# Kernel optimization log

Hardware: AMD Instinct MI355X
Metric: run time of the kernel (lower is better)

## Reference

```python
import jax, jax.numpy as jnp
import numpy as np

TSTEPS = 64
NEU_IN = 8192
NEU_OUT = 8192
DECAY = (2.0**4 - 1.0) / 2.0**4  # hyp.decay = 4 -> 0.9375
THRES = 1.0                      # hyp.mempot_thres


def setup_inputs() -> dict:
    key = jax.random.key(0)
    k1, k2 = jax.random.split(key)
    # input spike raster over all timesteps (sparse boolean events)
    spikes_in = jax.random.bernoulli(k1, 0.2, (TSTEPS, NEU_IN))
    # kaiming_normal_ init: std = sqrt(2 / fan_in)
    std = np.sqrt(2.0 / NEU_IN).astype(np.float32)
    weights = jax.random.normal(k2, (NEU_OUT, NEU_IN), dtype=jnp.float32) * std
    return {"spikes_in": spikes_in, "weights": weights}


def reference(spikes_in, weights):
    """LIF neuron layer scanned over timesteps.

    Per step (matches torch forward):
      mempot += W @ spikes_in[t]
      spike   = mempot >= THRES
      mempot -= THRES * spike
      mempot *= where(spike, 1, DECAY)
    Returns (spikes [TSTEPS+1, NEU_OUT] bool, final mempot [NEU_OUT]).
    """
    spikes_f = spikes_in.astype(jnp.float32)

    def step(mempot, s_in):
        m = mempot + weights @ s_in                      # GEMV [NEU_OUT]
        spike = m >= THRES
        sf = spike.astype(jnp.float32)
        m = (m - THRES * sf) * jnp.where(spike, 1.0, DECAY)
        return m, spike

    m0 = jnp.zeros((NEU_OUT,), jnp.float32)
    mempot_final, spikes = jax.lax.scan(step, m0, spikes_f)
    # torch stores into self.spikes[tstep + 1]; row 0 stays zero
    spikes_out = jnp.concatenate(
        [jnp.zeros((1, NEU_OUT), dtype=bool), spikes], axis=0
    )
    return spikes_out, mempot_final
```

## Files before the change

kernel.cpp:

```cpp
#include <hip/hip_runtime.h>

#define TSTEPS 64
#define NI 8192
#define NO 8192
#define KS 16
#define KCH (NI / KS)
#define DECAY 0.9375f

typedef __attribute__((ext_vector_type(8))) short bf16x8;
typedef __attribute__((ext_vector_type(4))) float f32x4;

__global__ __launch_bounds__(256) void convert_kernel(const void* sp,
                                                      unsigned short* __restrict__ Sbf) {
    __shared__ int any;
    if (threadIdx.x == 0) any = 0;
    __syncthreads();
    int local = 0;
    const unsigned int* win = (const unsigned int*)sp;
    #pragma unroll
    for (int i = 0; i < 4; ++i) {
        unsigned int v = win[threadIdx.x * 4 + i];
        if (v & 0xFFFFFF00u) local = 1;
    }
    if (local) atomicOr(&any, 1);
    __syncthreads();
    const int f = any;

    const int gid = blockIdx.x * 256 + threadIdx.x;
    const int t   = gid >> 10;
    const int k0  = (gid & 1023) * 8;
    unsigned h[8];
    #pragma unroll
    for (int e = 0; e < 8; ++e) {
        int gi = t * NI + k0 + e;
        bool b;
        if (f) b = ((const unsigned char*)sp)[gi] != 0;
        else   b = ((const int*)sp)[gi] != 0;
        h[e] = b ? 0x3F80u : 0u;
    }
    uint4 v;
    v.x = h[0] | (h[1] << 16);
    v.y = h[2] | (h[3] << 16);
    v.z = h[4] | (h[5] << 16);
    v.w = h[6] | (h[7] << 16);
    *(uint4*)(Sbf + (size_t)t * NI + k0) = v;
}

__device__ __forceinline__ void split3(const float4& x, const float4& y,
                                       bf16x8& hi, bf16x8& mid, bf16x8& lo) {
    float v[8] = {x.x, x.y, x.z, x.w, y.x, y.y, y.z, y.w};
    #pragma unroll
    for (int e = 0; e < 8; ++e) {
        unsigned b   = __float_as_uint(v[e]);
        unsigned hb  = b & 0xFFFF0000u;
        float    r1  = v[e] - __uint_as_float(hb);
        unsigned r1b = __float_as_uint(r1);
        unsigned mb  = r1b & 0xFFFF0000u;
        float    r2  = r1 - __uint_as_float(mb);
        unsigned r2b = __float_as_uint(r2);
        unsigned lr  = (r2b + 0x7FFFu + ((r2b >> 16) & 1u)) >> 16;
        hi[e]  = (short)(b >> 16);
        mid[e] = (short)(mb >> 16);
        lo[e]  = (short)lr;
    }
}

__device__ __forceinline__ void gload_lds16(const float* g, float* l) {
    __builtin_amdgcn_global_load_lds(
        (const __attribute__((address_space(1))) void*)g,
        (__attribute__((address_space(3))) void*)l, 16, 0, 0);
}

#define MFMA_BF16 __builtin_amdgcn_mfma_f32_16x16x32_bf16
#define WAIT8() do { asm volatile("s_waitcnt vmcnt(8)" ::: "memory"); \
                     __builtin_amdgcn_sched_barrier(0); } while (0)

__global__ __launch_bounds__(256, 4) void gemm_kernel(const float* __restrict__ W,
                                                      const unsigned short* __restrict__ Sbf,
                                                      float* __restrict__ partial) {
    __shared__ __align__(1024) float lds[8192];

    const int lane = threadIdx.x & 63;
    const int w    = threadIdx.x >> 6;
    const int ob   = blockIdx.x & 63;
    const int kb   = blockIdx.x >> 6;
    const int r16  = lane & 15;
    const int kg   = lane >> 4;
    const int o0   = ob * 128 + w * 32;
    const int kblk = kb * KCH;

    char* wlds = (char*)lds + w * 8192;

    const float* gw[2][2];
    #pragma unroll
    for (int m = 0; m < 2; ++m)
        #pragma unroll
        for (int j = 0; j < 2; ++j) {
            int row  = m * 16 + j * 8 + (lane >> 3);
            int usrc = (lane & 7) ^ ((lane >> 3) & 7);
            gw[m][j] = W + (size_t)(o0 + row) * NI + kblk + usrc * 4;
        }

    int offA[2][2];
    #pragma unroll
    for (int m = 0; m < 2; ++m)
        #pragma unroll
        for (int h = 0; h < 2; ++h)
            offA[m][h] = m * 2048 + r16 * 128 + (((kg * 2 + h) ^ (r16 & 7)) * 16);

    const unsigned short* bp[4];
    #pragma unroll
    for (int n = 0; n < 4; ++n)
        bp[n] = Sbf + (size_t)(n * 16 + r16) * NI + kblk + kg * 8;

    f32x4 acc[2][4];
    #pragma unroll
    for (int m = 0; m < 2; ++m)
        #pragma unroll
        for (int n = 0; n < 4; ++n) acc[m][n] = (f32x4)0.f;

    bf16x8 bX[4], bY[4];

    #define ISSUE_A(cc, stage) do {                                          \
        char* _d = wlds + (stage) * 4096;                                    \
        _Pragma("unroll") for (int m = 0; m < 2; ++m)                        \
        _Pragma("unroll") for (int j = 0; j < 2; ++j)                        \
            gload_lds16(gw[m][j] + (cc) * 32,                                \
                        (float*)(_d + m * 2048 + j * 1024));                 \
    } while (0)

    #define ISSUE_B(BB, cc) do {                                             \
        _Pragma("unroll") for (int n = 0; n < 4; ++n)                        \
            BB[n] = *(const bf16x8*)(bp[n] + (cc) * 32);                     \
    } while (0)

    #define COMPUTE(stage, BB) do {                                          \
        const char* _s = wlds + (stage) * 4096;                              \
        _Pragma("unroll") for (int m = 0; m < 2; ++m) {                      \
            float4 a0 = *(const float4*)(_s + offA[m][0]);                   \
            float4 a1 = *(const float4*)(_s + offA[m][1]);                   \
            bf16x8 hi, mid, lo;                                              \
            split3(a0, a1, hi, mid, lo);                                     \
            _Pragma("unroll") for (int n = 0; n < 4; ++n) {                  \
                acc[m][n] = MFMA_BF16(hi,  BB[n], acc[m][n], 0, 0, 0);       \
                acc[m][n] = MFMA_BF16(mid, BB[n], acc[m][n], 0, 0, 0);       \
                acc[m][n] = MFMA_BF16(lo,  BB[n], acc[m][n], 0, 0, 0);       \
            }                                                                \
        }                                                                    \
    } while (0)

    ISSUE_A(0, 0); ISSUE_B(bX, 0);
    ISSUE_A(1, 1); ISSUE_B(bY, 1);

    #pragma unroll 1
    for (int c = 0; c < 16; c += 2) {
        WAIT8();
        COMPUTE(0, bX);
        ISSUE_A((c + 2) & 15, 0); ISSUE_B(bX, (c + 2) & 15);
        WAIT8();
        COMPUTE(1, bY);
        ISSUE_A((c + 3) & 15, 1); ISSUE_B(bY, (c + 3) & 15);
    }

    #pragma unroll
    for (int m = 0; m < 2; ++m)
        #pragma unroll
        for (int n = 0; n < 4; ++n) {
            int t = n * 16 + r16;
            size_t off = (size_t)kb * TSTEPS * NO + (size_t)t * NO
                       + (o0 + m * 16 + kg * 4);
            *(f32x4*)&partial[off] = acc[m][n];
        }
}

__global__ __launch_bounds__(256) void reduce_kernel(const float* __restrict__ partial,
                                                     float* __restrict__ currents) {
    int gid = blockIdx.x * 256 + threadIdx.x;
    float s = 0.f;
    #pragma unroll
    for (int kb = 0; kb < KS; ++kb) s += partial[(size_t)kb * TSTEPS * NO + gid];
    currents[gid] = s;
}

__global__ __launch_bounds__(256) void scan_kernel(const float* __restrict__ currents,
                                                   float* __restrict__ out) {
    int o = blockIdx.x * 256 + threadIdx.x;
    float m = 0.f;
    out[o] = 0.f;
    for (int t = 0; t < TSTEPS; ++t) {
        m += currents[t * NO + o];
        bool sp = (m >= 1.0f);
        out[(size_t)(t + 1) * NO + o] = sp ? 1.0f : 0.0f;
        m = sp ? (m - 1.0f) : m * DECAY;
    }
    out[(size_t)(TSTEPS + 1) * NO + o] = m;
}

extern "C" void kernel_launch(void* const* d_in, const int* in_sizes, int n_in,
                              void* d_out, int out_size, void* d_ws, size_t ws_size,
                              hipStream_t stream) {
    const void*  spikes = d_in[0];
    const float* W      = (const float*)d_in[1];
    float*       out    = (float*)d_out;
    char*        ws     = (char*)d_ws;

    unsigned short* Sbf      = (unsigned short*)ws;
    float*          partial  = (float*)(ws + (size_t)1048576);
    float*          currents = (float*)(ws + (size_t)1048576
                                           + (size_t)KS * TSTEPS * NO * 4);

    hipLaunchKernelGGL(convert_kernel, dim3(256),               dim3(256), 0, stream,
                       spikes, Sbf);
    hipLaunchKernelGGL(gemm_kernel,    dim3(64 * KS),           dim3(256), 0, stream,
                       W, Sbf, partial);
    hipLaunchKernelGGL(reduce_kernel,  dim3(TSTEPS * NO / 256), dim3(256), 0, stream,
                       partial, currents);
    hipLaunchKernelGGL(scan_kernel,    dim3(NO / 256),          dim3(256), 0, stream,
                       currents, out);
}
```

Before: 97.43 us.

## Reduce split-K partials in LDS within block to shrink partial buffer traffic

```diff
diff --git a/kernel.cpp b/kernel.cpp
--- a/kernel.cpp
+++ b/kernel.cpp
@@ -3,8 +3,6 @@
 #define TSTEPS 64
 #define NI 8192
 #define NO 8192
-#define KS 16
-#define KCH (NI / KS)
 #define DECAY 0.9375f
 
 typedef __attribute__((ext_vector_type(8))) short bf16x8;
@@ -78,18 +76,19 @@
 __global__ __launch_bounds__(256, 4) void gemm_kernel(const float* __restrict__ W,
                                                       const unsigned short* __restrict__ Sbf,
                                                       float* __restrict__ partial) {
-    __shared__ __align__(1024) float lds[8192];
-
-    const int lane = threadIdx.x & 63;
-    const int w    = threadIdx.x >> 6;
-    const int ob   = blockIdx.x & 63;
-    const int kb   = blockIdx.x >> 6;
+    __shared__ __align__(1024) char smem[33280];
+
+    const int tid  = threadIdx.x;
+    const int lane = tid & 63;
+    const int w    = tid >> 6;
+    const int ob   = blockIdx.x >> 2;
+    const int kb   = blockIdx.x & 3;
     const int r16  = lane & 15;
     const int kg   = lane >> 4;
-    const int o0   = ob * 128 + w * 32;
-    const int kblk = kb * KCH;
-
-    char* wlds = (char*)lds + w * 8192;
+    const int o0   = ob * 32;
+    const int kblk = (kb * 4 + w) * 512;
+
+    char* wlds = smem + w * 8192;
 
     const float* gw[2][2];
     #pragma unroll
@@ -162,24 +161,34 @@
         ISSUE_A((c + 3) & 15, 1); ISSUE_B(bY, (c + 3) & 15);
     }
 
-    #pragma unroll
-    for (int m = 0; m < 2; ++m)
-        #pragma unroll
-        for (int n = 0; n < 4; ++n) {
-            int t = n * 16 + r16;
-            size_t off = (size_t)kb * TSTEPS * NO + (size_t)t * NO
-                       + (o0 + m * 16 + kg * 4);
-            *(f32x4*)&partial[off] = acc[m][n];
-        }
+    __syncthreads();
+    float (*red)[32][65] = (float (*)[32][65])smem;
+
+    #pragma unroll
+    for (int m = 0; m < 2; ++m)
+        #pragma unroll
+        for (int n = 0; n < 4; ++n)
+            #pragma unroll
+            for (int r = 0; r < 4; ++r)
+                red[w][m * 16 + kg * 4 + r][n * 16 + r16] = acc[m][n][r];
+    __syncthreads();
+
+    float* slice = partial + (size_t)blockIdx.x * 2048;
+    #pragma unroll
+    for (int j = 0; j < 8; ++j) {
+        int cell = j * 256 + tid;
+        int t = cell >> 5, o5 = cell & 31;
+        slice[cell] = red[0][o5][t] + red[1][o5][t] + red[2][o5][t] + red[3][o5][t];
+    }
 }
 
 __global__ __launch_bounds__(256) void reduce_kernel(const float* __restrict__ partial,
                                                      float* __restrict__ currents) {
     int gid = blockIdx.x * 256 + threadIdx.x;
-    float s = 0.f;
-    #pragma unroll
-    for (int kb = 0; kb < KS; ++kb) s += partial[(size_t)kb * TSTEPS * NO + gid];
-    currents[gid] = s;
+    int o = gid & (NO - 1);
+    int t = gid >> 13;
+    const float* base = partial + ((size_t)(o >> 5) * 4) * 2048 + t * 32 + (o & 31);
+    currents[gid] = base[0] + base[2048] + base[4096] + base[6144];
 }
 
 __global__ __launch_bounds__(256) void scan_kernel(const float* __restrict__ currents,
@@ -206,12 +215,11 @@
 
     unsigned short* Sbf      = (unsigned short*)ws;
     float*          partial  = (float*)(ws + (size_t)1048576);
-    float*          currents = (float*)(ws + (size_t)1048576
-                                           + (size_t)KS * TSTEPS * NO * 4);
+    float*          currents = (float*)(ws + (size_t)1048576 + (size_t)8388608);
 
     hipLaunchKernelGGL(convert_kernel, dim3(256),               dim3(256), 0, stream,
                        spikes, Sbf);
-    hipLaunchKernelGGL(gemm_kernel,    dim3(64 * KS),           dim3(256), 0, stream,
+    hipLaunchKernelGGL(gemm_kernel,    dim3(1024),              dim3(256), 0, stream,
                        W, Sbf, partial);
     hipLaunchKernelGGL(reduce_kernel,  dim3(TSTEPS * NO / 256), dim3(256), 0, stream,
                        partial, currents);
```

Result: faster. 80.33 us (-17.5%).
